# Kernel optimization log

Measured on AMD Instinct MI355X. Metric: run time of the kernel, lower is better.

## Reference

```python
import jax, jax.numpy as jnp
import numpy as np

N, M, D = 8192, 8192, 512

def setup_inputs() -> dict:
    key = jax.random.key(0)
    kx, ky = jax.random.split(key)
    x = jax.random.normal(kx, (N, D), dtype=jnp.float32)
    y = jax.random.normal(ky, (M, D), dtype=jnp.float32)
    gamma = jnp.ones((1,), dtype=jnp.float32)
    return {"x": x, "y": y, "gamma": gamma}

def reference(x, y, gamma):
    # Flatten leading dims as in the torch module
    x = x.reshape(-1, x.shape[-1])  # (N, D)
    y = y.reshape(-1, y.shape[-1])  # (M, D)
    x2 = jnp.sum(x * x, axis=-1)  # (N,)
    y2 = jnp.sum(y * y, axis=-1)  # (M,)
    xy = jnp.einsum('nd,md->nm', x, y)  # (N, M)
    sq_norm = x2[:, None] + y2[None, :] - 2.0 * xy
    return jnp.exp(-gamma[0] * sq_norm)
```

## Files before the change

kernel.cpp:

```cpp
#include <hip/hip_runtime.h>

#define NROWS 8192
#define DDIM  512
#define OUTN  8192

typedef int   i32x4 __attribute__((ext_vector_type(4)));
typedef int   i32x8 __attribute__((ext_vector_type(8)));
typedef float f32x4 __attribute__((ext_vector_type(4)));

__global__ void __launch_bounds__(256)
rbf_prep(const float* __restrict__ x, const float* __restrict__ y,
         unsigned char* __restrict__ xs, unsigned char* __restrict__ ys,
         float* __restrict__ x2, float* __restrict__ y2) {
    int wave = (blockIdx.x * blockDim.x + threadIdx.x) >> 6;
    int lane = threadIdx.x & 63;

    const float* src;
    unsigned char* dst;
    float* nrm;
    int row;
    if (wave < NROWS) { src = x; dst = xs; nrm = x2; row = wave; }
    else              { src = y; dst = ys; nrm = y2; row = wave - NROWS; }

    const float* p = src + (size_t)row * DDIM + lane * 8;
    float4 v0 = *(const float4*)(p);
    float4 v1 = *(const float4*)(p + 4);

    float s = v0.x * v0.x + v0.y * v0.y + v0.z * v0.z + v0.w * v0.w
            + v1.x * v1.x + v1.y * v1.y + v1.z * v1.z + v1.w * v1.w;

    int lo = __builtin_amdgcn_cvt_pk_fp8_f32(v0.x, v0.y, 0, false);
    lo     = __builtin_amdgcn_cvt_pk_fp8_f32(v0.z, v0.w, lo, true);
    int hi = __builtin_amdgcn_cvt_pk_fp8_f32(v1.x, v1.y, 0, false);
    hi     = __builtin_amdgcn_cvt_pk_fp8_f32(v1.z, v1.w, hi, true);

    int h  = lane >> 4;
    int kq = (lane >> 2) & 3;
    int kb = (lane & 3) * 8;
    size_t off = (size_t)(row >> 4) * 8192 + h * 2048 + kq * 512
               + (row & 15) * 32 + kb;
    *(int2*)(dst + off) = make_int2(lo, hi);

#pragma unroll
    for (int off2 = 32; off2 > 0; off2 >>= 1) s += __shfl_down(s, off2, 64);
    if (lane == 0) nrm[row] = s;
}

__global__ void __launch_bounds__(256)
rbf_gemm(const unsigned char* __restrict__ xs,
         const unsigned char* __restrict__ ys,
         const float* __restrict__ x2, const float* __restrict__ y2,
         const float* __restrict__ gamma, float* __restrict__ out) {
    const int tid  = threadIdx.x;
    const int lane = tid & 63;
    const int w    = tid >> 6;
    const int wm   = w & 1;
    const int wn   = w >> 1;

    const int bm = blockIdx.x & 63;
    const int bn = blockIdx.x >> 6;
    const int row0 = bm * 128;
    const int col0 = bn * 128;

    f32x4 acc[4][4] = {};

    const unsigned char* abase = xs + (size_t)(bm * 8 + wm * 4) * 8192 + lane * 32;
    const unsigned char* bbase = ys + (size_t)(bn * 8 + wn * 4) * 8192 + lane * 32;

#pragma unroll 2
    for (int h = 0; h < 4; ++h) {
        i32x8 af[4], bfr[4];
#pragma unroll
        for (int mi = 0; mi < 4; ++mi) {
            const unsigned char* p = abase + mi * 8192 + h * 2048;
            i32x4 lo = *(const i32x4*)(p);
            i32x4 hi = *(const i32x4*)(p + 16);
            af[mi] = __builtin_shufflevector(lo, hi, 0, 1, 2, 3, 4, 5, 6, 7);
        }
#pragma unroll
        for (int ni = 0; ni < 4; ++ni) {
            const unsigned char* p = bbase + ni * 8192 + h * 2048;
            i32x4 lo = *(const i32x4*)(p);
            i32x4 hi = *(const i32x4*)(p + 16);
            bfr[ni] = __builtin_shufflevector(lo, hi, 0, 1, 2, 3, 4, 5, 6, 7);
        }
#pragma unroll
        for (int mi = 0; mi < 4; ++mi)
#pragma unroll
            for (int ni = 0; ni < 4; ++ni)
                acc[mi][ni] = __builtin_amdgcn_mfma_scale_f32_16x16x128_f8f6f4(
                    af[mi], bfr[ni], acc[mi][ni],
                    0, 0,
                    0, 0x7F,
                    0, 0x7F);
    }

    const float g = gamma[0];
#pragma unroll
    for (int mi = 0; mi < 4; ++mi) {
        const int rbase = row0 + wm * 64 + mi * 16 + (lane >> 4) * 4;
        float xn[4];
#pragma unroll
        for (int r = 0; r < 4; ++r) xn[r] = x2[rbase + r];
#pragma unroll
        for (int ni = 0; ni < 4; ++ni) {
            const int col = col0 + wn * 64 + ni * 16 + (lane & 15);
            const float yn = y2[col];
            float* op = out + (size_t)rbase * OUTN + col;
#pragma unroll
            for (int r = 0; r < 4; ++r) {
                float s = xn[r] + yn - 2.0f * acc[mi][ni][r];
                op[(size_t)r * OUTN] = __expf(-g * s);
            }
        }
    }
}

extern "C" void kernel_launch(void* const* d_in, const int* in_sizes, int n_in,
                              void* d_out, int out_size, void* d_ws, size_t ws_size,
                              hipStream_t stream) {
    const float* x     = (const float*)d_in[0];
    const float* y     = (const float*)d_in[1];
    const float* gamma = (const float*)d_in[2];
    float* out = (float*)d_out;

    char* ws = (char*)d_ws;
    unsigned char* xs = (unsigned char*)ws;
    unsigned char* ys = (unsigned char*)(ws + (size_t)NROWS * DDIM);
    float* x2 = (float*)(ws + (size_t)NROWS * DDIM * 2);
    float* y2 = (float*)(ws + (size_t)NROWS * DDIM * 2 + NROWS * 4);

    rbf_prep<<<4096, 256, 0, stream>>>(x, y, xs, ys, x2, y2);
    rbf_gemm<<<4096, 256, 0, stream>>>(xs, ys, x2, y2, gamma, out);
}
```

Measured before the change: 315.9 us.

## Switch to 32x32x64 FP8 MFMA with a repacked layout and nontemporal stores

```diff
diff --git a/kernel.cpp b/kernel.cpp
--- a/kernel.cpp
+++ b/kernel.cpp
@@ -4,49 +4,58 @@
 #define DDIM  512
 #define OUTN  8192
 
-typedef int   i32x4 __attribute__((ext_vector_type(4)));
-typedef int   i32x8 __attribute__((ext_vector_type(8)));
-typedef float f32x4 __attribute__((ext_vector_type(4)));
+typedef int   i32x4  __attribute__((ext_vector_type(4)));
+typedef int   i32x8  __attribute__((ext_vector_type(8)));
+typedef float f32x16 __attribute__((ext_vector_type(16)));
 
 __global__ void __launch_bounds__(256)
 rbf_prep(const float* __restrict__ x, const float* __restrict__ y,
          unsigned char* __restrict__ xs, unsigned char* __restrict__ ys,
          float* __restrict__ x2, float* __restrict__ y2) {
-    int wave = (blockIdx.x * blockDim.x + threadIdx.x) >> 6;
-    int lane = threadIdx.x & 63;
+    __shared__ unsigned char lbuf[16384];
+    const int tid  = threadIdx.x;
+    const int lane = tid & 63;
+    const int w    = tid >> 6;
 
-    const float* src;
-    unsigned char* dst;
-    float* nrm;
-    int row;
-    if (wave < NROWS) { src = x; dst = xs; nrm = x2; row = wave; }
-    else              { src = y; dst = ys; nrm = y2; row = wave - NROWS; }
+    int grp = blockIdx.x;
+    const float* src; unsigned char* dst; float* nrm;
+    if (grp < 256) { src = x; dst = xs; nrm = x2; }
+    else           { grp -= 256; src = y; dst = ys; nrm = y2; }
 
-    const float* p = src + (size_t)row * DDIM + lane * 8;
-    float4 v0 = *(const float4*)(p);
-    float4 v1 = *(const float4*)(p + 4);
-
-    float s = v0.x * v0.x + v0.y * v0.y + v0.z * v0.z + v0.w * v0.w
-            + v1.x * v1.x + v1.y * v1.y + v1.z * v1.z + v1.w * v1.w;
-
-    int lo = __builtin_amdgcn_cvt_pk_fp8_f32(v0.x, v0.y, 0, false);
-    lo     = __builtin_amdgcn_cvt_pk_fp8_f32(v0.z, v0.w, lo, true);
-    int hi = __builtin_amdgcn_cvt_pk_fp8_f32(v1.x, v1.y, 0, false);
-    hi     = __builtin_amdgcn_cvt_pk_fp8_f32(v1.z, v1.w, hi, true);
-
-    int h  = lane >> 4;
-    int kq = (lane >> 2) & 3;
-    int kb = (lane & 3) * 8;
-    size_t off = (size_t)(row >> 4) * 8192 + h * 2048 + kq * 512
-               + (row & 15) * 32 + kb;
-    *(int2*)(dst + off) = make_int2(lo, hi);
+    const int loff_base = (lane >> 3) * 2048 + ((lane >> 2) & 1) * 1024 + (lane & 3) * 8;
 
 #pragma unroll
-    for (int off2 = 32; off2 > 0; off2 >>= 1) s += __shfl_down(s, off2, 64);
-    if (lane == 0) nrm[row] = s;
+    for (int j = 0; j < 8; ++j) {
+        const int r   = w * 8 + j;
+        const int row = grp * 32 + r;
+        const float* p = src + (size_t)row * DDIM + lane * 8;
+        float4 v0 = *(const float4*)(p);
+        float4 v1 = *(const float4*)(p + 4);
+
+        float s = v0.x * v0.x + v0.y * v0.y + v0.z * v0.z + v0.w * v0.w
+                + v1.x * v1.x + v1.y * v1.y + v1.z * v1.z + v1.w * v1.w;
+
+        int lo = __builtin_amdgcn_cvt_pk_fp8_f32(v0.x, v0.y, 0, false);
+        lo     = __builtin_amdgcn_cvt_pk_fp8_f32(v0.z, v0.w, lo, true);
+        int hi = __builtin_amdgcn_cvt_pk_fp8_f32(v1.x, v1.y, 0, false);
+        hi     = __builtin_amdgcn_cvt_pk_fp8_f32(v1.z, v1.w, hi, true);
+
+        *(int2*)(lbuf + loff_base + r * 32) = make_int2(lo, hi);
+
+#pragma unroll
+        for (int o = 32; o > 0; o >>= 1) s += __shfl_down(s, o, 64);
+        if (lane == 0) nrm[row] = s;
+    }
+
+    __syncthreads();
+    unsigned char* gdst = dst + (size_t)grp * 16384;
+#pragma unroll
+    for (int it = 0; it < 4; ++it)
+        *(i32x4*)(gdst + it * 4096 + tid * 16) =
+            *(const i32x4*)(lbuf + it * 4096 + tid * 16);
 }
 
-__global__ void __launch_bounds__(256)
+__global__ void __launch_bounds__(256, 3)
 rbf_gemm(const unsigned char* __restrict__ xs,
          const unsigned char* __restrict__ ys,
          const float* __restrict__ x2, const float* __restrict__ y2,
@@ -62,55 +71,59 @@
     const int row0 = bm * 128;
     const int col0 = bn * 128;
 
-    f32x4 acc[4][4] = {};
+    f32x16 acc[2][2] = {};
 
-    const unsigned char* abase = xs + (size_t)(bm * 8 + wm * 4) * 8192 + lane * 32;
-    const unsigned char* bbase = ys + (size_t)(bn * 8 + wn * 4) * 8192 + lane * 32;
+    const unsigned char* abase = xs + (size_t)(bm * 4 + wm * 2) * 16384 + lane * 32;
+    const unsigned char* bbase = ys + (size_t)(bn * 4 + wn * 2) * 16384 + lane * 32;
 
 #pragma unroll 2
-    for (int h = 0; h < 4; ++h) {
-        i32x8 af[4], bfr[4];
+    for (int h = 0; h < 8; ++h) {
+        i32x8 af[2], bf[2];
 #pragma unroll
-        for (int mi = 0; mi < 4; ++mi) {
-            const unsigned char* p = abase + mi * 8192 + h * 2048;
+        for (int mi = 0; mi < 2; ++mi) {
+            const unsigned char* p = abase + mi * 16384 + h * 2048;
             i32x4 lo = *(const i32x4*)(p);
             i32x4 hi = *(const i32x4*)(p + 16);
             af[mi] = __builtin_shufflevector(lo, hi, 0, 1, 2, 3, 4, 5, 6, 7);
         }
 #pragma unroll
-        for (int ni = 0; ni < 4; ++ni) {
-            const unsigned char* p = bbase + ni * 8192 + h * 2048;
+        for (int ni = 0; ni < 2; ++ni) {
+            const unsigned char* p = bbase + ni * 16384 + h * 2048;
             i32x4 lo = *(const i32x4*)(p);
             i32x4 hi = *(const i32x4*)(p + 16);
-            bfr[ni] = __builtin_shufflevector(lo, hi, 0, 1, 2, 3, 4, 5, 6, 7);
+            bf[ni] = __builtin_shufflevector(lo, hi, 0, 1, 2, 3, 4, 5, 6, 7);
         }
 #pragma unroll
-        for (int mi = 0; mi < 4; ++mi)
+        for (int mi = 0; mi < 2; ++mi)
 #pragma unroll
-            for (int ni = 0; ni < 4; ++ni)
-                acc[mi][ni] = __builtin_amdgcn_mfma_scale_f32_16x16x128_f8f6f4(
-                    af[mi], bfr[ni], acc[mi][ni],
+            for (int ni = 0; ni < 2; ++ni)
+                acc[mi][ni] = __builtin_amdgcn_mfma_scale_f32_32x32x64_f8f6f4(
+                    af[mi], bf[ni], acc[mi][ni],
                     0, 0,
                     0, 0x7F,
                     0, 0x7F);
     }
 
-    const float g = gamma[0];
+    const float g  = gamma[0];
+    const int   rq = (lane >> 5) * 4;
+    const int   cl = lane & 31;
 #pragma unroll
-    for (int mi = 0; mi < 4; ++mi) {
-        const int rbase = row0 + wm * 64 + mi * 16 + (lane >> 4) * 4;
-        float xn[4];
+    for (int mi = 0; mi < 2; ++mi) {
+        const int rbase = row0 + wm * 64 + mi * 32;
+        float xn[16];
 #pragma unroll
-        for (int r = 0; r < 4; ++r) xn[r] = x2[rbase + r];
+        for (int r = 0; r < 16; ++r)
+            xn[r] = x2[rbase + (r & 3) + 8 * (r >> 2) + rq];
 #pragma unroll
-        for (int ni = 0; ni < 4; ++ni) {
-            const int col = col0 + wn * 64 + ni * 16 + (lane & 15);
+        for (int ni = 0; ni < 2; ++ni) {
+            const int col = col0 + wn * 64 + ni * 32 + cl;
             const float yn = y2[col];
-            float* op = out + (size_t)rbase * OUTN + col;
 #pragma unroll
-            for (int r = 0; r < 4; ++r) {
-                float s = xn[r] + yn - 2.0f * acc[mi][ni][r];
-                op[(size_t)r * OUTN] = __expf(-g * s);
+            for (int r = 0; r < 16; ++r) {
+                const int row = rbase + (r & 3) + 8 * (r >> 2) + rq;
+                const float s = xn[r] + yn - 2.0f * acc[mi][ni][r];
+                __builtin_nontemporal_store(__expf(-g * s),
+                                            out + (size_t)row * OUTN + col);
             }
         }
     }
@@ -130,6 +143,6 @@
     float* x2 = (float*)(ws + (size_t)NROWS * DDIM * 2);
     float* y2 = (float*)(ws + (size_t)NROWS * DDIM * 2 + NROWS * 4);
 
-    rbf_prep<<<4096, 256, 0, stream>>>(x, y, xs, ys, x2, y2);
+    rbf_prep<<<512, 256, 0, stream>>>(x, y, xs, ys, x2, y2);
     rbf_gemm<<<4096, 256, 0, stream>>>(xs, ys, x2, y2, gamma, out);
 }
```

Result: faster. 303.8 us (-3.8%).
